# Optimization experiments

Hardware: AMD Instinct MI355X
Metric: run time of the kernel (lower is better)

Reference implementation:

```python
import jax, jax.numpy as jnp
import numpy as np

IN_FEATURES = 4096
OUT_FEATURES = 11008


def setup_inputs() -> dict:
    key = jax.random.key(0)
    kx, kw, ks, kb = jax.random.split(key, 4)
    x = jax.random.normal(kx, (64, IN_FEATURES), dtype=jnp.float32)
    # int8 quantized weight, stored as int32 for portability (values in [-128, 127])
    weight_quantized = jax.random.randint(kw, (OUT_FEATURES, IN_FEATURES), -128, 128, dtype=jnp.int32)
    # per-tensor scale, as produced by quantize_weights_int8: |w|.max()/127
    weight_scale = jnp.asarray(0.01, dtype=jnp.float32)
    bias = jax.random.normal(kb, (OUT_FEATURES,), dtype=jnp.float32) * 0.02
    return {"x": x, "weight_quantized": weight_quantized, "weight_scale": weight_scale, "bias": bias}


def reference(x, weight_quantized, weight_scale, bias):
    # dequantize_weights_int8: q.float() * scale, then F.linear(x, W, b) = x @ W.T + b
    weight = weight_quantized.astype(jnp.float32) * weight_scale  # [out, in]
    return jnp.einsum('mi,oi->mo', x, weight) + bias
```

## Files before the change

### kernel.cpp

```cpp
#include <hip/hip_runtime.h>
#include <hip/hip_bf16.h>


#define M_DIM 64
#define N_DIM 11008
#define K_DIM 4096
#define KSPLIT 8
#define KC (K_DIM / KSPLIT)
#define BK 128
#define LDS_STRIDE 136
#define BLOCK_N 64

typedef __attribute__((ext_vector_type(8))) short bf16x8;
typedef __attribute__((ext_vector_type(4))) float f32x4;
typedef __attribute__((ext_vector_type(4))) int i32x4;
typedef __attribute__((ext_vector_type(4))) short s16x4;

__device__ __forceinline__ short i2bf(int q) {
    float f = (float)q;
    return (short)(__builtin_bit_cast(unsigned int, f) >> 16);
}

__device__ __forceinline__ short f2bf(float f) {
    unsigned int u = __builtin_bit_cast(unsigned int, f);
    u = u + 0x7FFFu + ((u >> 16) & 1u);
    return (short)(u >> 16);
}


__global__ __launch_bounds__(256) void qlinear_partial_kernel(const float* __restrict__ x,
                                                              const int* __restrict__ wq,
                                                              const float* __restrict__ scale_p,
                                                              float* __restrict__ part) {
    __shared__ short lds[M_DIM * LDS_STRIDE];

    const int tid  = threadIdx.x;
    const int wave = tid >> 6;
    const int lane = tid & 63;
    const int quad = lane >> 4;
    const int l16  = lane & 15;

    const int n0  = blockIdx.x * BLOCK_N;
    const int kc0 = blockIdx.y * KC;
    const float scale = *scale_p;

    const int nw = n0 + wave * 16 + l16;
    const int* wptr = wq + (size_t)nw * K_DIM + kc0 + quad * 8;

    f32x4 acc[4] = {f32x4{0,0,0,0}, f32x4{0,0,0,0}, f32x4{0,0,0,0}, f32x4{0,0,0,0}};

    for (int kb = 0; kb < KC; kb += BK) {
        {
            const float* xbase = x + kc0 + kb;
            #pragma unroll
            for (int j = 0; j < 8; ++j) {
                int f  = tid + j * 256;
                int row = f >> 5;
                int c4  = f & 31;
                f32x4 v = *(const f32x4*)(xbase + (size_t)row * K_DIM + c4 * 4);
                s16x4 h;
                h.x = f2bf(v.x); h.y = f2bf(v.y); h.z = f2bf(v.z); h.w = f2bf(v.w);
                *(s16x4*)&lds[row * LDS_STRIDE + c4 * 4] = h;
            }
        }
        __syncthreads();

        #pragma unroll
        for (int kk = 0; kk < BK; kk += 32) {
            i32x4 b0 = *(const i32x4*)(wptr + kb + kk);
            i32x4 b1 = *(const i32x4*)(wptr + kb + kk + 4);
            bf16x8 bfrag;
            bfrag[0] = i2bf(b0.x); bfrag[1] = i2bf(b0.y);
            bfrag[2] = i2bf(b0.z); bfrag[3] = i2bf(b0.w);
            bfrag[4] = i2bf(b1.x); bfrag[5] = i2bf(b1.y);
            bfrag[6] = i2bf(b1.z); bfrag[7] = i2bf(b1.w);

            #pragma unroll
            for (int mi = 0; mi < 4; ++mi) {
                bf16x8 afrag = *(const bf16x8*)&lds[(mi * 16 + l16) * LDS_STRIDE + kk + quad * 8];
                acc[mi] = __builtin_amdgcn_mfma_f32_16x16x32_bf16(afrag, bfrag, acc[mi], 0, 0, 0);
            }
        }
        __syncthreads();
    }

    float* dst = part + (size_t)blockIdx.y * ((size_t)M_DIM * N_DIM);
    const int nout = n0 + wave * 16 + l16;
    #pragma unroll
    for (int mi = 0; mi < 4; ++mi) {
        #pragma unroll
        for (int r = 0; r < 4; ++r) {
            int m = mi * 16 + quad * 4 + r;
            dst[(size_t)m * N_DIM + nout] = acc[mi][r] * scale;
        }
    }
}

__global__ __launch_bounds__(256) void reduce_bias_kernel(const float* __restrict__ part,
                                                          const float* __restrict__ bias,
                                                          float* __restrict__ out) {
    size_t idx  = (size_t)blockIdx.x * 256 + threadIdx.x;
    int    col4 = (int)(idx % (N_DIM / 4));
    f32x4 s = *(const f32x4*)(bias + col4 * 4);
    #pragma unroll
    for (int p = 0; p < KSPLIT; ++p) {
        f32x4 v = *(const f32x4*)(part + (size_t)p * M_DIM * N_DIM + idx * 4);
        s.x += v.x; s.y += v.y; s.z += v.z; s.w += v.w;
    }
    *(f32x4*)(out + idx * 4) = s;
}


__global__ __launch_bounds__(256) void init_bias_kernel(const float* __restrict__ bias,
                                                        float* __restrict__ out) {
    int idx = blockIdx.x * 256 + threadIdx.x;
    int col4 = idx % 2752;
    f32x4 b = *(const f32x4*)(bias + col4 * 4);
    *(f32x4*)(out + (size_t)idx * 4) = b;
}

__global__ __launch_bounds__(256) void qlinear_atomic_kernel(const float* __restrict__ x,
                                                             const int* __restrict__ wq,
                                                             const float* __restrict__ scale_p,
                                                             float* __restrict__ out) {
    __shared__ short lds[M_DIM * LDS_STRIDE];

    const int tid  = threadIdx.x;
    const int wave = tid >> 6;
    const int lane = tid & 63;
    const int quad = lane >> 4;
    const int l16  = lane & 15;

    const int n0  = blockIdx.x * BLOCK_N;
    const int kc0 = blockIdx.y * KC;
    const float scale = *scale_p;

    const int nw = n0 + wave * 16 + l16;
    const int* wptr = wq + (size_t)nw * K_DIM + kc0 + quad * 8;

    f32x4 acc[4] = {f32x4{0,0,0,0}, f32x4{0,0,0,0}, f32x4{0,0,0,0}, f32x4{0,0,0,0}};

    for (int kb = 0; kb < KC; kb += BK) {
        {
            const float* xbase = x + kc0 + kb;
            #pragma unroll
            for (int j = 0; j < 8; ++j) {
                int f  = tid + j * 256;
                int row = f >> 5;
                int c4  = f & 31;
                f32x4 v = *(const f32x4*)(xbase + (size_t)row * K_DIM + c4 * 4);
                s16x4 h;
                h.x = f2bf(v.x); h.y = f2bf(v.y); h.z = f2bf(v.z); h.w = f2bf(v.w);
                *(s16x4*)&lds[row * LDS_STRIDE + c4 * 4] = h;
            }
        }
        __syncthreads();

        #pragma unroll
        for (int kk = 0; kk < BK; kk += 32) {
            i32x4 b0 = *(const i32x4*)(wptr + kb + kk);
            i32x4 b1 = *(const i32x4*)(wptr + kb + kk + 4);
            bf16x8 bfrag;
            bfrag[0] = i2bf(b0.x); bfrag[1] = i2bf(b0.y);
            bfrag[2] = i2bf(b0.z); bfrag[3] = i2bf(b0.w);
            bfrag[4] = i2bf(b1.x); bfrag[5] = i2bf(b1.y);
            bfrag[6] = i2bf(b1.z); bfrag[7] = i2bf(b1.w);

            #pragma unroll
            for (int mi = 0; mi < 4; ++mi) {
                bf16x8 afrag = *(const bf16x8*)&lds[(mi * 16 + l16) * LDS_STRIDE + kk + quad * 8];
                acc[mi] = __builtin_amdgcn_mfma_f32_16x16x32_bf16(afrag, bfrag, acc[mi], 0, 0, 0);
            }
        }
        __syncthreads();
    }

    const int nout = n0 + wave * 16 + l16;
    #pragma unroll
    for (int mi = 0; mi < 4; ++mi) {
        #pragma unroll
        for (int r = 0; r < 4; ++r) {
            int m = mi * 16 + quad * 4 + r;
            atomicAdd(&out[(size_t)m * N_DIM + nout], acc[mi][r] * scale);
        }
    }
}

extern "C" void kernel_launch(void* const* d_in, const int* in_sizes, int n_in,
                              void* d_out, int out_size, void* d_ws, size_t ws_size,
                              hipStream_t stream) {
    const float* x      = (const float*)d_in[0];
    const int*   wq     = (const int*)d_in[1];
    const float* scale  = (const float*)d_in[2];
    const float* bias   = (const float*)d_in[3];
    float* out = (float*)d_out;

    const size_t part_bytes = (size_t)KSPLIT * M_DIM * N_DIM * sizeof(float);
    dim3 grid(N_DIM / BLOCK_N, KSPLIT);

    if (ws_size >= part_bytes && d_ws != nullptr) {
        float* part = (float*)d_ws;
        qlinear_partial_kernel<<<grid, 256, 0, stream>>>(x, wq, scale, part);
        reduce_bias_kernel<<<(M_DIM * N_DIM / 4) / 256, 256, 0, stream>>>(part, bias, out);
    } else {
        init_bias_kernel<<<688, 256, 0, stream>>>(bias, out);
        qlinear_atomic_kernel<<<grid, 256, 0, stream>>>(x, wq, scale, out);
    }
}
```

Measured before the change: 263.1 us.

## Pre-convert x to bf16 and fuse split-K reduction and bias into one kernel

Adds a small kernel that converts x to bf16 once into the workspace. Each block of the main kernel now owns 16 output columns and splits K across its 4 waves, reducing the partials in LDS and applying scale and bias before writing the output directly. This removes the large split-K partial buffer write and read and the separate reduce pass. The cost is that A fragments are now read straight from global/L2 with no LDS staging, and each block covers fewer columns.

```diff
diff --git a/kernel.cpp b/kernel.cpp
--- a/kernel.cpp
+++ b/kernel.cpp
@@ -1,17 +1,15 @@
 #include <hip/hip_runtime.h>
-#include <hip/hip_bf16.h>
 
 
 #define M_DIM 64
 #define N_DIM 11008
 #define K_DIM 4096
-#define KSPLIT 8
-#define KC (K_DIM / KSPLIT)
-#define BK 128
-#define LDS_STRIDE 136
-#define BLOCK_N 64
+#define BLOCK_N 16
+#define NBLOCKS (N_DIM / BLOCK_N)
+#define KW (K_DIM / 4)
 
 typedef __attribute__((ext_vector_type(8))) short bf16x8;
+typedef __attribute__((ext_vector_type(8))) short s16x8;
 typedef __attribute__((ext_vector_type(4))) float f32x4;
 typedef __attribute__((ext_vector_type(4))) int i32x4;
 typedef __attribute__((ext_vector_type(4))) short s16x4;
@@ -27,12 +25,23 @@
     return (short)(u >> 16);
 }
 
-
-__global__ __launch_bounds__(256) void qlinear_partial_kernel(const float* __restrict__ x,
-                                                              const int* __restrict__ wq,
-                                                              const float* __restrict__ scale_p,
-                                                              float* __restrict__ part) {
-    __shared__ short lds[M_DIM * LDS_STRIDE];
+__global__ __launch_bounds__(256) void xcvt_kernel(const float* __restrict__ x,
+                                                   short* __restrict__ xbf) {
+    int idx = (blockIdx.x * 256 + threadIdx.x) * 8;
+    f32x4 a = *(const f32x4*)(x + idx);
+    f32x4 b = *(const f32x4*)(x + idx + 4);
+    s16x8 h;
+    h[0] = f2bf(a.x); h[1] = f2bf(a.y); h[2] = f2bf(a.z); h[3] = f2bf(a.w);
+    h[4] = f2bf(b.x); h[5] = f2bf(b.y); h[6] = f2bf(b.z); h[7] = f2bf(b.w);
+    *(s16x8*)(xbf + idx) = h;
+}
+
+__global__ __launch_bounds__(256) void qlinear_fused_kernel(const short* __restrict__ xbf,
+                                                            const int* __restrict__ wq,
+                                                            const float* __restrict__ scale_p,
+                                                            const float* __restrict__ bias,
+                                                            float* __restrict__ out) {
+    __shared__ float red[4][M_DIM][BLOCK_N];
 
     const int tid  = threadIdx.x;
     const int wave = tid >> 6;
@@ -40,7 +49,87 @@
     const int quad = lane >> 4;
     const int l16  = lane & 15;
 
-    const int n0  = blockIdx.x * BLOCK_N;
+    const int n0 = blockIdx.x * BLOCK_N;
+    const int k0 = wave * KW;
+
+    const int*   bptr = wq  + (size_t)(n0 + l16) * K_DIM + k0 + quad * 8;
+    const short* aptr = xbf + (size_t)l16 * K_DIM + k0 + quad * 8;
+
+    f32x4 acc[4] = {f32x4{0,0,0,0}, f32x4{0,0,0,0}, f32x4{0,0,0,0}, f32x4{0,0,0,0}};
+
+    #pragma unroll 4
+    for (int kk = 0; kk < KW; kk += 32) {
+        i32x4 b0 = *(const i32x4*)(bptr + kk);
+        i32x4 b1 = *(const i32x4*)(bptr + kk + 4);
+        bf16x8 bfrag;
+        bfrag[0] = i2bf(b0.x); bfrag[1] = i2bf(b0.y);
+        bfrag[2] = i2bf(b0.z); bfrag[3] = i2bf(b0.w);
+        bfrag[4] = i2bf(b1.x); bfrag[5] = i2bf(b1.y);
+        bfrag[6] = i2bf(b1.z); bfrag[7] = i2bf(b1.w);
+
+        #pragma unroll
+        for (int mi = 0; mi < 4; ++mi) {
+            bf16x8 afrag = *(const bf16x8*)(aptr + (size_t)mi * 16 * K_DIM + kk);
+            acc[mi] = __builtin_amdgcn_mfma_f32_16x16x32_bf16(afrag, bfrag, acc[mi], 0, 0, 0);
+        }
+    }
+
+    #pragma unroll
+    for (int mi = 0; mi < 4; ++mi) {
+        #pragma unroll
+        for (int r = 0; r < 4; ++r) {
+            red[wave][mi * 16 + quad * 4 + r][l16] = acc[mi][r];
+        }
+    }
+    __syncthreads();
+
+    {
+        const float scale = *scale_p;
+        int idx = tid * 4;
+        int m = idx >> 4;
+        int n = idx & 15;
+        f32x4 s0 = *(const f32x4*)&red[0][m][n];
+        f32x4 s1 = *(const f32x4*)&red[1][m][n];
+        f32x4 s2 = *(const f32x4*)&red[2][m][n];
+        f32x4 s3 = *(const f32x4*)&red[3][m][n];
+        f32x4 bb = *(const f32x4*)(bias + n0 + n);
+        f32x4 r;
+        r.x = (s0.x + s1.x + s2.x + s3.x) * scale + bb.x;
+        r.y = (s0.y + s1.y + s2.y + s3.y) * scale + bb.y;
+        r.z = (s0.z + s1.z + s2.z + s3.z) * scale + bb.z;
+        r.w = (s0.w + s1.w + s2.w + s3.w) * scale + bb.w;
+        *(f32x4*)(out + (size_t)m * N_DIM + n0 + n) = r;
+    }
+}
+
+
+#define KSPLIT 8
+#define KC (K_DIM / KSPLIT)
+#define BK 128
+#define LDS_STRIDE 136
+#define FB_BLOCK_N 64
+
+__global__ __launch_bounds__(256) void init_bias_kernel(const float* __restrict__ bias,
+                                                        float* __restrict__ out) {
+    int idx = blockIdx.x * 256 + threadIdx.x;
+    int col4 = idx % 2752;
+    f32x4 b = *(const f32x4*)(bias + col4 * 4);
+    *(f32x4*)(out + (size_t)idx * 4) = b;
+}
+
+__global__ __launch_bounds__(256) void qlinear_atomic_kernel(const float* __restrict__ x,
+                                                             const int* __restrict__ wq,
+                                                             const float* __restrict__ scale_p,
+                                                             float* __restrict__ out) {
+    __shared__ short lds[M_DIM * LDS_STRIDE];
+
+    const int tid  = threadIdx.x;
+    const int wave = tid >> 6;
+    const int lane = tid & 63;
+    const int quad = lane >> 4;
+    const int l16  = lane & 15;
+
+    const int n0  = blockIdx.x * FB_BLOCK_N;
     const int kc0 = blockIdx.y * KC;
     const float scale = *scale_p;
 
@@ -84,97 +173,6 @@
         __syncthreads();
     }
 
-    float* dst = part + (size_t)blockIdx.y * ((size_t)M_DIM * N_DIM);
-    const int nout = n0 + wave * 16 + l16;
-    #pragma unroll
-    for (int mi = 0; mi < 4; ++mi) {
-        #pragma unroll
-        for (int r = 0; r < 4; ++r) {
-            int m = mi * 16 + quad * 4 + r;
-            dst[(size_t)m * N_DIM + nout] = acc[mi][r] * scale;
-        }
-    }
-}
-
-__global__ __launch_bounds__(256) void reduce_bias_kernel(const float* __restrict__ part,
-                                                          const float* __restrict__ bias,
-                                                          float* __restrict__ out) {
-    size_t idx  = (size_t)blockIdx.x * 256 + threadIdx.x;
-    int    col4 = (int)(idx % (N_DIM / 4));
-    f32x4 s = *(const f32x4*)(bias + col4 * 4);
-    #pragma unroll
-    for (int p = 0; p < KSPLIT; ++p) {
-        f32x4 v = *(const f32x4*)(part + (size_t)p * M_DIM * N_DIM + idx * 4);
-        s.x += v.x; s.y += v.y; s.z += v.z; s.w += v.w;
-    }
-    *(f32x4*)(out + idx * 4) = s;
-}
-
-
-__global__ __launch_bounds__(256) void init_bias_kernel(const float* __restrict__ bias,
-                                                        float* __restrict__ out) {
-    int idx = blockIdx.x * 256 + threadIdx.x;
-    int col4 = idx % 2752;
-    f32x4 b = *(const f32x4*)(bias + col4 * 4);
-    *(f32x4*)(out + (size_t)idx * 4) = b;
-}
-
-__global__ __launch_bounds__(256) void qlinear_atomic_kernel(const float* __restrict__ x,
-                                                             const int* __restrict__ wq,
-                                                             const float* __restrict__ scale_p,
-                                                             float* __restrict__ out) {
-    __shared__ short lds[M_DIM * LDS_STRIDE];
-
-    const int tid  = threadIdx.x;
-    const int wave = tid >> 6;
-    const int lane = tid & 63;
-    const int quad = lane >> 4;
-    const int l16  = lane & 15;
-
-    const int n0  = blockIdx.x * BLOCK_N;
-    const int kc0 = blockIdx.y * KC;
-    const float scale = *scale_p;
-
-    const int nw = n0 + wave * 16 + l16;
-    const int* wptr = wq + (size_t)nw * K_DIM + kc0 + quad * 8;
-
-    f32x4 acc[4] = {f32x4{0,0,0,0}, f32x4{0,0,0,0}, f32x4{0,0,0,0}, f32x4{0,0,0,0}};
-
-    for (int kb = 0; kb < KC; kb += BK) {
-        {
-            const float* xbase = x + kc0 + kb;
-            #pragma unroll
-            for (int j = 0; j < 8; ++j) {
-                int f  = tid + j * 256;
-                int row = f >> 5;
-                int c4  = f & 31;
-                f32x4 v = *(const f32x4*)(xbase + (size_t)row * K_DIM + c4 * 4);
-                s16x4 h;
-                h.x = f2bf(v.x); h.y = f2bf(v.y); h.z = f2bf(v.z); h.w = f2bf(v.w);
-                *(s16x4*)&lds[row * LDS_STRIDE + c4 * 4] = h;
-            }
-        }
-        __syncthreads();
-
-        #pragma unroll
-        for (int kk = 0; kk < BK; kk += 32) {
-            i32x4 b0 = *(const i32x4*)(wptr + kb + kk);
-            i32x4 b1 = *(const i32x4*)(wptr + kb + kk + 4);
-            bf16x8 bfrag;
-            bfrag[0] = i2bf(b0.x); bfrag[1] = i2bf(b0.y);
-            bfrag[2] = i2bf(b0.z); bfrag[3] = i2bf(b0.w);
-            bfrag[4] = i2bf(b1.x); bfrag[5] = i2bf(b1.y);
-            bfrag[6] = i2bf(b1.z); bfrag[7] = i2bf(b1.w);
-
-            #pragma unroll
-            for (int mi = 0; mi < 4; ++mi) {
-                bf16x8 afrag = *(const bf16x8*)&lds[(mi * 16 + l16) * LDS_STRIDE + kk + quad * 8];
-                acc[mi] = __builtin_amdgcn_mfma_f32_16x16x32_bf16(afrag, bfrag, acc[mi], 0, 0, 0);
-            }
-        }
-        __syncthreads();
-    }
-
     const int nout = n0 + wave * 16 + l16;
     #pragma unroll
     for (int mi = 0; mi < 4; ++mi) {
@@ -195,15 +193,15 @@
     const float* bias   = (const float*)d_in[3];
     float* out = (float*)d_out;
 
-    const size_t part_bytes = (size_t)KSPLIT * M_DIM * N_DIM * sizeof(float);
-    dim3 grid(N_DIM / BLOCK_N, KSPLIT);
-
-    if (ws_size >= part_bytes && d_ws != nullptr) {
-        float* part = (float*)d_ws;
-        qlinear_partial_kernel<<<grid, 256, 0, stream>>>(x, wq, scale, part);
-        reduce_bias_kernel<<<(M_DIM * N_DIM / 4) / 256, 256, 0, stream>>>(part, bias, out);
+    const size_t xbf_bytes = (size_t)M_DIM * K_DIM * sizeof(short);
+
+    if (ws_size >= xbf_bytes && d_ws != nullptr) {
+        short* xbf = (short*)d_ws;
+        xcvt_kernel<<<(M_DIM * K_DIM) / (256 * 8), 256, 0, stream>>>(x, xbf);
+        qlinear_fused_kernel<<<NBLOCKS, 256, 0, stream>>>(xbf, wq, scale, bias, out);
     } else {
         init_bias_kernel<<<688, 256, 0, stream>>>(bias, out);
+        dim3 grid(N_DIM / FB_BLOCK_N, KSPLIT);
         qlinear_atomic_kernel<<<grid, 256, 0, stream>>>(x, wq, scale, out);
     }
 }
```

Result: slower. 285.2 us (+8.4%).

## Stage weights via direct global-to-LDS loads, pre-convert x to bf16, use atomics

Applied to the files above, without the earlier changes.

Adds a pre-pass kernel that converts x to bf16 once into the workspace. The main kernel then loads both weight and x tiles straight into swizzled LDS using global_load_lds, instead of per-thread register loads and conversions. The split-K partial buffer and its reduction kernel are replaced by a bias init followed by atomicAdd accumulation, which cuts partial-buffer traffic but adds atomic contention and an extra launch. Staging is not double-buffered, so the loads are not overlapped with the MFMA work.

```diff
diff --git a/kernel.cpp b/kernel.cpp
--- a/kernel.cpp
+++ b/kernel.cpp
@@ -1,5 +1,4 @@
 #include <hip/hip_runtime.h>
-#include <hip/hip_bf16.h>
 
 
 #define M_DIM 64
@@ -8,10 +7,10 @@
 #define KSPLIT 8
 #define KC (K_DIM / KSPLIT)
 #define BK 128
-#define LDS_STRIDE 136
 #define BLOCK_N 64
 
 typedef __attribute__((ext_vector_type(8))) short bf16x8;
+typedef __attribute__((ext_vector_type(8))) short s16x8;
 typedef __attribute__((ext_vector_type(4))) float f32x4;
 typedef __attribute__((ext_vector_type(4))) int i32x4;
 typedef __attribute__((ext_vector_type(4))) short s16x4;
@@ -27,11 +26,110 @@
     return (short)(u >> 16);
 }
 
-
-__global__ __launch_bounds__(256) void qlinear_partial_kernel(const float* __restrict__ x,
-                                                              const int* __restrict__ wq,
-                                                              const float* __restrict__ scale_p,
-                                                              float* __restrict__ part) {
+__device__ __forceinline__ void load_lds_16B(const void* g, void* l) {
+    __builtin_amdgcn_global_load_lds(
+        (const __attribute__((address_space(1))) unsigned int*)g,
+        (__attribute__((address_space(3))) unsigned int*)l,
+        16, 0, 0);
+}
+
+__global__ __launch_bounds__(256) void xcvt_kernel(const float* __restrict__ x,
+                                                   short* __restrict__ xbf) {
+    int idx = (blockIdx.x * 256 + threadIdx.x) * 8;
+    f32x4 a = *(const f32x4*)(x + idx);
+    f32x4 b = *(const f32x4*)(x + idx + 4);
+    s16x8 h;
+    h[0] = f2bf(a.x); h[1] = f2bf(a.y); h[2] = f2bf(a.z); h[3] = f2bf(a.w);
+    h[4] = f2bf(b.x); h[5] = f2bf(b.y); h[6] = f2bf(b.z); h[7] = f2bf(b.w);
+    *(s16x8*)(xbf + idx) = h;
+}
+
+__global__ __launch_bounds__(256) void init_bias_kernel(const float* __restrict__ bias,
+                                                        float* __restrict__ out) {
+    int idx = blockIdx.x * 256 + threadIdx.x;
+    int col4 = idx % 2752;
+    f32x4 b = *(const f32x4*)(bias + col4 * 4);
+    *(f32x4*)(out + (size_t)idx * 4) = b;
+}
+
+__global__ __launch_bounds__(256) void qlinear_v4_kernel(const short* __restrict__ xbf,
+                                                         const int* __restrict__ wq,
+                                                         const float* __restrict__ scale_p,
+                                                         float* __restrict__ out) {
+    __shared__ char smem[49152];
+    char* wlds = smem;
+    char* xlds = smem + 32768;
+
+    const int tid  = threadIdx.x;
+    const int wave = tid >> 6;
+    const int lane = tid & 63;
+    const int quad = lane >> 4;
+    const int l16  = lane & 15;
+
+    const int n0  = blockIdx.x * BLOCK_N;
+    const int kc0 = blockIdx.y * KC;
+    const float scale = *scale_p;
+
+    f32x4 acc[4] = {f32x4{0,0,0,0}, f32x4{0,0,0,0}, f32x4{0,0,0,0}, f32x4{0,0,0,0}};
+
+    for (int kb = 0; kb < KC; kb += BK) {
+        #pragma unroll
+        for (int j = 0; j < 8; ++j) {
+            int row  = wave * 16 + j * 2 + (lane >> 5);
+            int colb = ((lane & 31) * 16) ^ ((row & 7) << 4);
+            const char* g = (const char*)(wq + (size_t)(n0 + row) * K_DIM + kc0 + kb) + colb;
+            load_lds_16B(g, wlds + (wave * 16 + j * 2) * 512);
+        }
+        #pragma unroll
+        for (int j = 0; j < 4; ++j) {
+            int row  = wave * 16 + j * 4 + (lane >> 4);
+            int colb = ((lane & 15) * 16) ^ ((row & 7) << 4);
+            const char* g = (const char*)(xbf + (size_t)row * K_DIM + kc0 + kb) + colb;
+            load_lds_16B(g, xlds + (wave * 16 + j * 4) * 256);
+        }
+        __syncthreads();
+
+        #pragma unroll
+        for (int kk = 0; kk < BK; kk += 32) {
+            const int wrow = wave * 16 + l16;
+            const int wsw  = (wrow & 7) << 4;
+            const int L0   = (kk + quad * 8) * 4;
+            i32x4 b0 = *(const i32x4*)(wlds + wrow * 512 + ((L0)      ^ wsw));
+            i32x4 b1 = *(const i32x4*)(wlds + wrow * 512 + ((L0 + 16) ^ wsw));
+            bf16x8 bfrag;
+            bfrag[0] = i2bf(b0.x); bfrag[1] = i2bf(b0.y);
+            bfrag[2] = i2bf(b0.z); bfrag[3] = i2bf(b0.w);
+            bfrag[4] = i2bf(b1.x); bfrag[5] = i2bf(b1.y);
+            bfrag[6] = i2bf(b1.z); bfrag[7] = i2bf(b1.w);
+
+            #pragma unroll
+            for (int mi = 0; mi < 4; ++mi) {
+                const int arow = mi * 16 + l16;
+                const int La   = (kk + quad * 8) * 2;
+                bf16x8 afrag = *(const bf16x8*)(xlds + arow * 256 + (La ^ ((arow & 7) << 4)));
+                acc[mi] = __builtin_amdgcn_mfma_f32_16x16x32_bf16(afrag, bfrag, acc[mi], 0, 0, 0);
+            }
+        }
+        __syncthreads();
+    }
+
+    const int nout = n0 + wave * 16 + l16;
+    #pragma unroll
+    for (int mi = 0; mi < 4; ++mi) {
+        #pragma unroll
+        for (int r = 0; r < 4; ++r) {
+            int m = mi * 16 + quad * 4 + r;
+            atomicAdd(&out[(size_t)m * N_DIM + nout], acc[mi][r] * scale);
+        }
+    }
+}
+
+#define LDS_STRIDE 136
+
+__global__ __launch_bounds__(256) void qlinear_atomic_kernel(const float* __restrict__ x,
+                                                             const int* __restrict__ wq,
+                                                             const float* __restrict__ scale_p,
+                                                             float* __restrict__ out) {
     __shared__ short lds[M_DIM * LDS_STRIDE];
 
     const int tid  = threadIdx.x;
@@ -84,97 +182,6 @@
         __syncthreads();
     }
 
-    float* dst = part + (size_t)blockIdx.y * ((size_t)M_DIM * N_DIM);
-    const int nout = n0 + wave * 16 + l16;
-    #pragma unroll
-    for (int mi = 0; mi < 4; ++mi) {
-        #pragma unroll
-        for (int r = 0; r < 4; ++r) {
-            int m = mi * 16 + quad * 4 + r;
-            dst[(size_t)m * N_DIM + nout] = acc[mi][r] * scale;
-        }
-    }
-}
-
-__global__ __launch_bounds__(256) void reduce_bias_kernel(const float* __restrict__ part,
-                                                          const float* __restrict__ bias,
-                                                          float* __restrict__ out) {
-    size_t idx  = (size_t)blockIdx.x * 256 + threadIdx.x;
-    int    col4 = (int)(idx % (N_DIM / 4));
-    f32x4 s = *(const f32x4*)(bias + col4 * 4);
-    #pragma unroll
-    for (int p = 0; p < KSPLIT; ++p) {
-        f32x4 v = *(const f32x4*)(part + (size_t)p * M_DIM * N_DIM + idx * 4);
-        s.x += v.x; s.y += v.y; s.z += v.z; s.w += v.w;
-    }
-    *(f32x4*)(out + idx * 4) = s;
-}
-
-
-__global__ __launch_bounds__(256) void init_bias_kernel(const float* __restrict__ bias,
-                                                        float* __restrict__ out) {
-    int idx = blockIdx.x * 256 + threadIdx.x;
-    int col4 = idx % 2752;
-    f32x4 b = *(const f32x4*)(bias + col4 * 4);
-    *(f32x4*)(out + (size_t)idx * 4) = b;
-}
-
-__global__ __launch_bounds__(256) void qlinear_atomic_kernel(const float* __restrict__ x,
-                                                             const int* __restrict__ wq,
-                                                             const float* __restrict__ scale_p,
-                                                             float* __restrict__ out) {
-    __shared__ short lds[M_DIM * LDS_STRIDE];
-
-    const int tid  = threadIdx.x;
-    const int wave = tid >> 6;
-    const int lane = tid & 63;
-    const int quad = lane >> 4;
-    const int l16  = lane & 15;
-
-    const int n0  = blockIdx.x * BLOCK_N;
-    const int kc0 = blockIdx.y * KC;
-    const float scale = *scale_p;
-
-    const int nw = n0 + wave * 16 + l16;
-    const int* wptr = wq + (size_t)nw * K_DIM + kc0 + quad * 8;
-
-    f32x4 acc[4] = {f32x4{0,0,0,0}, f32x4{0,0,0,0}, f32x4{0,0,0,0}, f32x4{0,0,0,0}};
-
-    for (int kb = 0; kb < KC; kb += BK) {
-        {
-            const float* xbase = x + kc0 + kb;
-            #pragma unroll
-            for (int j = 0; j < 8; ++j) {
-                int f  = tid + j * 256;
-                int row = f >> 5;
-                int c4  = f & 31;
-                f32x4 v = *(const f32x4*)(xbase + (size_t)row * K_DIM + c4 * 4);
-                s16x4 h;
-                h.x = f2bf(v.x); h.y = f2bf(v.y); h.z = f2bf(v.z); h.w = f2bf(v.w);
-                *(s16x4*)&lds[row * LDS_STRIDE + c4 * 4] = h;
-            }
-        }
-        __syncthreads();
-
-        #pragma unroll
-        for (int kk = 0; kk < BK; kk += 32) {
-            i32x4 b0 = *(const i32x4*)(wptr + kb + kk);
-            i32x4 b1 = *(const i32x4*)(wptr + kb + kk + 4);
-            bf16x8 bfrag;
-            bfrag[0] = i2bf(b0.x); bfrag[1] = i2bf(b0.y);
-            bfrag[2] = i2bf(b0.z); bfrag[3] = i2bf(b0.w);
-            bfrag[4] = i2bf(b1.x); bfrag[5] = i2bf(b1.y);
-            bfrag[6] = i2bf(b1.z); bfrag[7] = i2bf(b1.w);
-
-            #pragma unroll
-            for (int mi = 0; mi < 4; ++mi) {
-                bf16x8 afrag = *(const bf16x8*)&lds[(mi * 16 + l16) * LDS_STRIDE + kk + quad * 8];
-                acc[mi] = __builtin_amdgcn_mfma_f32_16x16x32_bf16(afrag, bfrag, acc[mi], 0, 0, 0);
-            }
-        }
-        __syncthreads();
-    }
-
     const int nout = n0 + wave * 16 + l16;
     #pragma unroll
     for (int mi = 0; mi < 4; ++mi) {
@@ -195,13 +202,14 @@
     const float* bias   = (const float*)d_in[3];
     float* out = (float*)d_out;
 
-    const size_t part_bytes = (size_t)KSPLIT * M_DIM * N_DIM * sizeof(float);
+    const size_t xbf_bytes = (size_t)M_DIM * K_DIM * sizeof(short);
     dim3 grid(N_DIM / BLOCK_N, KSPLIT);
 
-    if (ws_size >= part_bytes && d_ws != nullptr) {
-        float* part = (float*)d_ws;
-        qlinear_partial_kernel<<<grid, 256, 0, stream>>>(x, wq, scale, part);
-        reduce_bias_kernel<<<(M_DIM * N_DIM / 4) / 256, 256, 0, stream>>>(part, bias, out);
+    if (ws_size >= xbf_bytes && d_ws != nullptr) {
+        short* xbf = (short*)d_ws;
+        xcvt_kernel<<<(M_DIM * K_DIM) / (256 * 8), 256, 0, stream>>>(x, xbf);
+        init_bias_kernel<<<688, 256, 0, stream>>>(bias, out);
+        qlinear_v4_kernel<<<grid, 256, 0, stream>>>(xbf, wq, scale, out);
     } else {
         init_bias_kernel<<<688, 256, 0, stream>>>(bias, out);
         qlinear_atomic_kernel<<<grid, 256, 0, stream>>>(x, wq, scale, out);
```

New measurement: 259.2 us (median of 2 runs). About the same (-1.5%).
